# Kernel tuning notes

Hardware: AMD Instinct MI355X
Metric: run time of the kernel (lower is better)

The kernel has to match this reference:

```python
import jax, jax.numpy as jnp
import numpy as np
from jax import lax

BLOCK_SIZE = 5
GAMMA = 0.02


def setup_inputs() -> dict:
    key = jax.random.key(0)
    kx, km = jax.random.split(key)
    N, C, H, W = 64, 64, 80, 80
    x = jax.random.normal(kx, (N, C, H, W), dtype=jnp.float32)
    # Bernoulli(gamma) sample, materialized as an int32 0/1 mask (the module's
    # internal randomness, fixed for deterministic reference comparison).
    mask = (jax.random.uniform(km, (N, C, H, W)) < GAMMA).astype(jnp.int32)
    return {"x": x, "mask": mask}


def _dropblock(x, mask, block_size):
    m = mask.astype(x.dtype)  # 0/1 seed mask, shape (N,C,H,W)
    # Original scatters each seed (h,w) into [h, h+bs) x [w, w+bs) (clipped at
    # H,W). Equivalent dense form: block_mask[i,j] = max over m[i-dh, j-dw],
    # dh,dw in [0,bs) -> sliding-window max with top/left padding of bs-1.
    if block_size > 1:
        block_mask = lax.reduce_window(
            m,
            jnp.array(0.0, x.dtype),
            lax.max,
            window_dimensions=(1, 1, block_size, block_size),
            window_strides=(1, 1, 1, 1),
            padding=((0, 0), (0, 0), (block_size - 1, 0), (block_size - 1, 0)),
        )
    else:
        block_mask = m
    inv_blk_mask = 1.0 - block_mask
    countM = jnp.array(m.size, x.dtype)
    count_ones = inv_blk_mask.sum()
    return inv_blk_mask * x * (countM / count_ones)


def reference(x, mask):
    return _dropblock(x, mask, BLOCK_SIZE)
```

## Files before the change

### kernel.cpp

```cpp
#include <hip/hip_runtime.h>

#define DB_H 80
#define DB_W 80
#define DB_PLANE (DB_H * DB_W)
#define DB_NPLANES 4096
#define DB_ROW_WORDS 3
#define DB_PLANE_WORDS (DB_H * DB_ROW_WORDS)
#define DB_TOTAL (DB_PLANE * DB_NPLANES)
#define DB_COUNT_F 26214400.0f
#define DB_CNT_BYTES (DB_NPLANES * 4)
#define WPB 4

__global__ __launch_bounds__(256) void db_mask_kernel(
    const int* __restrict__ mask,
    unsigned int* __restrict__ bits,
    unsigned int* __restrict__ counts)
{
    __shared__ unsigned long long P[WPB][104];
    __shared__ unsigned int RO[WPB][DB_PLANE_WORDS];
    const int wid = threadIdx.x >> 6, lane = threadIdx.x & 63;
    const int plane = blockIdx.x * WPB + wid;
    const int* mp = mask + plane * DB_PLANE;
    unsigned long long* Pp = P[wid];
    unsigned int* ro = RO[wid];

    #pragma unroll
    for (int c = 0; c < 4; ++c) {
        int v[25];
        #pragma unroll
        for (int k = 0; k < 25; ++k) v[k] = mp[(c * 25 + k) * 64 + lane];
        #pragma unroll
        for (int k = 0; k < 25; ++k) {
            unsigned long long bal = __ballot(v[k] & 1);
            if (lane == 0) Pp[c * 25 + k] = bal;
        }
    }
    if (lane < 4) Pp[100 + lane] = 0ULL;
    __syncthreads();

    for (int r = lane; r < DB_H; r += 64) {
        const int bitpos = r * DB_W;
        const int q = bitpos >> 6, off = bitpos & 63;
        unsigned long long a, b;
        if (off) {
            a = (Pp[q] >> off) | (Pp[q + 1] << (64 - off));
            b = (Pp[q + 1] >> off) | (Pp[q + 2] << (64 - off));
        } else {
            a = Pp[q]; b = Pp[q + 1];
        }
        b &= 0xFFFFULL;
        unsigned long long ra = a, rb = b;
        #pragma unroll
        for (int s = 1; s <= 4; ++s) {
            ra |= a << s;
            rb |= (b << s) | (a >> (64 - s));
        }
        rb &= 0xFFFFULL;
        ro[r * 3 + 0] = (unsigned int)ra;
        ro[r * 3 + 1] = (unsigned int)(ra >> 32);
        ro[r * 3 + 2] = (unsigned int)rb;
    }
    __syncthreads();

    unsigned int zeros = 0;
    for (int i = lane; i < DB_H; i += 64) {
        const int lo = (i >= 4) ? i - 4 : 0;
        unsigned int c0 = 0, c1 = 0, c2 = 0;
        for (int ii = lo; ii <= i; ++ii) {
            c0 |= ro[ii * 3 + 0];
            c1 |= ro[ii * 3 + 1];
            c2 |= ro[ii * 3 + 2];
        }
        zeros += 80u - __popc(c0) - __popc(c1) - __popc(c2);
        unsigned int* bp = bits + plane * DB_PLANE_WORDS + i * 3;
        bp[0] = c0; bp[1] = c1; bp[2] = c2;
    }
    for (int off = 32; off > 0; off >>= 1)
        zeros += (unsigned int)__shfl_down((int)zeros, off, 64);
    if (lane == 0) counts[plane] = zeros;
}

__global__ __launch_bounds__(256) void db_apply_bits(
    const float4* __restrict__ x,
    const unsigned int* __restrict__ bits,
    const unsigned int* __restrict__ counts,
    float4* __restrict__ out)
{
    __shared__ float s_scale;
    __shared__ unsigned int s_part[4];
    {
        const uint4* cp = (const uint4*)counts;
        unsigned int c = 0;
        #pragma unroll
        for (int k = 0; k < 4; ++k) {
            uint4 v = cp[k * 256 + threadIdx.x];
            c += v.x + v.y + v.z + v.w;
        }
        for (int off = 32; off > 0; off >>= 1)
            c += (unsigned int)__shfl_down((int)c, off, 64);
        if ((threadIdx.x & 63) == 0) s_part[threadIdx.x >> 6] = c;
        __syncthreads();
        if (threadIdx.x == 0)
            s_scale = DB_COUNT_F /
                      (float)(s_part[0] + s_part[1] + s_part[2] + s_part[3]);
        __syncthreads();
    }
    const float scale = s_scale;
    const int NG = DB_TOTAL / 4;
    const int stride = gridDim.x * blockDim.x;
    #pragma unroll 2
    for (int g = blockIdx.x * blockDim.x + threadIdx.x; g < NG; g += stride) {
        float4 v = x[g];
        int e = g * 4;
        int plane = e / DB_PLANE;
        int ep = e - plane * DB_PLANE;
        int i = ep / DB_W;
        int j = ep - i * DB_W;
        unsigned int wb =
            bits[plane * DB_PLANE_WORDS + i * 3 + (j >> 5)] >> (j & 31);
        float4 o;
        o.x = (wb & 1u) ? 0.0f : v.x * scale;
        o.y = (wb & 2u) ? 0.0f : v.y * scale;
        o.z = (wb & 4u) ? 0.0f : v.z * scale;
        o.w = (wb & 8u) ? 0.0f : v.w * scale;
        out[g] = o;
    }
}

__global__ __launch_bounds__(256) void db_count_kernel(
    const int* __restrict__ mask,
    unsigned int* __restrict__ counts)
{
    __shared__ unsigned long long P[WPB][104];
    __shared__ unsigned int RO[WPB][DB_PLANE_WORDS];
    const int wid = threadIdx.x >> 6, lane = threadIdx.x & 63;
    const int plane = blockIdx.x * WPB + wid;
    const int* mp = mask + plane * DB_PLANE;
    unsigned long long* Pp = P[wid];
    unsigned int* ro = RO[wid];
    #pragma unroll
    for (int c = 0; c < 4; ++c) {
        int v[25];
        #pragma unroll
        for (int k = 0; k < 25; ++k) v[k] = mp[(c * 25 + k) * 64 + lane];
        #pragma unroll
        for (int k = 0; k < 25; ++k) {
            unsigned long long bal = __ballot(v[k] & 1);
            if (lane == 0) Pp[c * 25 + k] = bal;
        }
    }
    if (lane < 4) Pp[100 + lane] = 0ULL;
    __syncthreads();
    for (int r = lane; r < DB_H; r += 64) {
        const int bitpos = r * DB_W;
        const int q = bitpos >> 6, off = bitpos & 63;
        unsigned long long a, b;
        if (off) {
            a = (Pp[q] >> off) | (Pp[q + 1] << (64 - off));
            b = (Pp[q + 1] >> off) | (Pp[q + 2] << (64 - off));
        } else {
            a = Pp[q]; b = Pp[q + 1];
        }
        b &= 0xFFFFULL;
        unsigned long long ra = a, rb = b;
        #pragma unroll
        for (int s = 1; s <= 4; ++s) {
            ra |= a << s;
            rb |= (b << s) | (a >> (64 - s));
        }
        rb &= 0xFFFFULL;
        ro[r * 3 + 0] = (unsigned int)ra;
        ro[r * 3 + 1] = (unsigned int)(ra >> 32);
        ro[r * 3 + 2] = (unsigned int)rb;
    }
    __syncthreads();
    unsigned int zeros = 0;
    for (int i = lane; i < DB_H; i += 64) {
        const int lo = (i >= 4) ? i - 4 : 0;
        unsigned int c0 = 0, c1 = 0, c2 = 0;
        for (int ii = lo; ii <= i; ++ii) {
            c0 |= ro[ii * 3 + 0];
            c1 |= ro[ii * 3 + 1];
            c2 |= ro[ii * 3 + 2];
        }
        zeros += 80u - __popc(c0) - __popc(c1) - __popc(c2);
    }
    for (int off = 32; off > 0; off >>= 1)
        zeros += (unsigned int)__shfl_down((int)zeros, off, 64);
    if (lane == 0) counts[plane] = zeros;
}

__global__ __launch_bounds__(256) void db_apply_recompute(
    const float* __restrict__ x,
    const int* __restrict__ mask,
    const unsigned int* __restrict__ counts,
    float* __restrict__ out)
{
    __shared__ unsigned long long P[WPB][104];
    __shared__ unsigned int RO[WPB][DB_PLANE_WORDS];
    __shared__ unsigned int BM[WPB][DB_PLANE_WORDS];
    __shared__ float s_scale;
    __shared__ unsigned int s_part[4];
    {
        const uint4* cp = (const uint4*)counts;
        unsigned int c = 0;
        #pragma unroll
        for (int k = 0; k < 4; ++k) {
            uint4 v = cp[k * 256 + threadIdx.x];
            c += v.x + v.y + v.z + v.w;
        }
        for (int off = 32; off > 0; off >>= 1)
            c += (unsigned int)__shfl_down((int)c, off, 64);
        if ((threadIdx.x & 63) == 0) s_part[threadIdx.x >> 6] = c;
        __syncthreads();
        if (threadIdx.x == 0)
            s_scale = DB_COUNT_F /
                      (float)(s_part[0] + s_part[1] + s_part[2] + s_part[3]);
        __syncthreads();
    }
    const float scale = s_scale;
    const int wid = threadIdx.x >> 6, lane = threadIdx.x & 63;
    const int plane = blockIdx.x * WPB + wid;
    const int* mp = mask + plane * DB_PLANE;
    unsigned long long* Pp = P[wid];
    unsigned int* ro = RO[wid];
    #pragma unroll
    for (int c = 0; c < 4; ++c) {
        int v[25];
        #pragma unroll
        for (int k = 0; k < 25; ++k) v[k] = mp[(c * 25 + k) * 64 + lane];
        #pragma unroll
        for (int k = 0; k < 25; ++k) {
            unsigned long long bal = __ballot(v[k] & 1);
            if (lane == 0) Pp[c * 25 + k] = bal;
        }
    }
    if (lane < 4) Pp[100 + lane] = 0ULL;
    __syncthreads();
    for (int r = lane; r < DB_H; r += 64) {
        const int bitpos = r * DB_W;
        const int q = bitpos >> 6, off = bitpos & 63;
        unsigned long long a, b;
        if (off) {
            a = (Pp[q] >> off) | (Pp[q + 1] << (64 - off));
            b = (Pp[q + 1] >> off) | (Pp[q + 2] << (64 - off));
        } else {
            a = Pp[q]; b = Pp[q + 1];
        }
        b &= 0xFFFFULL;
        unsigned long long ra = a, rb = b;
        #pragma unroll
        for (int s = 1; s <= 4; ++s) {
            ra |= a << s;
            rb |= (b << s) | (a >> (64 - s));
        }
        rb &= 0xFFFFULL;
        ro[r * 3 + 0] = (unsigned int)ra;
        ro[r * 3 + 1] = (unsigned int)(ra >> 32);
        ro[r * 3 + 2] = (unsigned int)rb;
    }
    __syncthreads();
    unsigned int* bmp = BM[wid];
    for (int i = lane; i < DB_H; i += 64) {
        const int lo = (i >= 4) ? i - 4 : 0;
        unsigned int c0 = 0, c1 = 0, c2 = 0;
        for (int ii = lo; ii <= i; ++ii) {
            c0 |= ro[ii * 3 + 0];
            c1 |= ro[ii * 3 + 1];
            c2 |= ro[ii * 3 + 2];
        }
        bmp[i * 3 + 0] = c0; bmp[i * 3 + 1] = c1; bmp[i * 3 + 2] = c2;
    }
    __syncthreads();
    const float* xp = x + plane * DB_PLANE;
    float* op = out + plane * DB_PLANE;
    for (int e = lane; e < DB_PLANE; e += 64) {
        int i = e / DB_W, j = e - i * DB_W;
        unsigned int wb = bmp[i * 3 + (j >> 5)] >> (j & 31);
        op[e] = (wb & 1u) ? 0.0f : xp[e] * scale;
    }
}

extern "C" void kernel_launch(void* const* d_in, const int* in_sizes, int n_in,
                              void* d_out, int out_size, void* d_ws, size_t ws_size,
                              hipStream_t stream) {
    const float* x = (const float*)d_in[0];
    const int* mask = (const int*)d_in[1];
    float* out = (float*)d_out;

    unsigned int* counts = (unsigned int*)d_ws;
    unsigned int* bits = (unsigned int*)((char*)d_ws + DB_CNT_BYTES);
    const size_t bits_bytes = (size_t)DB_NPLANES * DB_PLANE_WORDS * 4;
    const bool use_bits = ws_size >= DB_CNT_BYTES + bits_bytes;

    if (use_bits) {
        db_mask_kernel<<<DB_NPLANES / WPB, 256, 0, stream>>>(mask, bits, counts);
        db_apply_bits<<<2048, 256, 0, stream>>>(
            (const float4*)x, bits, counts, (float4*)out);
    } else {
        db_count_kernel<<<DB_NPLANES / WPB, 256, 0, stream>>>(mask, counts);
        db_apply_recompute<<<DB_NPLANES / WPB, 256, 0, stream>>>(
            x, mask, counts, out);
    }
}
```

Baseline: 66.11 us.

## Split each plane across two waves and skip x loads for fully masked quads

The mask kernel now gives each plane to two wavefronts, each handling half the rows, with a shared-memory combine of the zero counts. This doubles the block count and lowers register use by shrinking the load unroll. The apply kernel skips reading x when all four elements of a float4 are masked, saving some read bandwidth. The fallback kernels also get smaller unroll chunks. The cost is an extra barrier and a divergent load in the apply loop.

```diff
diff --git a/kernel.cpp b/kernel.cpp
--- a/kernel.cpp
+++ b/kernel.cpp
@@ -9,6 +9,7 @@
 #define DB_TOTAL (DB_PLANE * DB_NPLANES)
 #define DB_COUNT_F 26214400.0f
 #define DB_CNT_BYTES (DB_NPLANES * 4)
+#define PPBLK 2
 #define WPB 4
 
 __global__ __launch_bounds__(256) void db_mask_kernel(
@@ -16,29 +17,34 @@
     unsigned int* __restrict__ bits,
     unsigned int* __restrict__ counts)
 {
-    __shared__ unsigned long long P[WPB][104];
-    __shared__ unsigned int RO[WPB][DB_PLANE_WORDS];
-    const int wid = threadIdx.x >> 6, lane = threadIdx.x & 63;
-    const int plane = blockIdx.x * WPB + wid;
+    __shared__ unsigned long long P[PPBLK][104];
+    __shared__ unsigned int RO[PPBLK][DB_PLANE_WORDS];
+    __shared__ unsigned int ZP[PPBLK][2];
+    const int t = threadIdx.x;
+    const int wid = t >> 6, lane = t & 63;
+    const int pib = wid >> 1, half = wid & 1;
+    const int plane = blockIdx.x * PPBLK + pib;
     const int* mp = mask + plane * DB_PLANE;
-    unsigned long long* Pp = P[wid];
-    unsigned int* ro = RO[wid];
-
-    #pragma unroll
-    for (int c = 0; c < 4; ++c) {
-        int v[25];
-        #pragma unroll
-        for (int k = 0; k < 25; ++k) v[k] = mp[(c * 25 + k) * 64 + lane];
-        #pragma unroll
-        for (int k = 0; k < 25; ++k) {
+    unsigned long long* Pp = P[pib];
+    unsigned int* ro = RO[pib];
+
+    #pragma unroll 1
+    for (int c = 0; c < 5; ++c) {
+        int v[10];
+        const int base = half * 50 + c * 10;
+        #pragma unroll
+        for (int k = 0; k < 10; ++k) v[k] = mp[(base + k) * 64 + lane];
+        #pragma unroll
+        for (int k = 0; k < 10; ++k) {
             unsigned long long bal = __ballot(v[k] & 1);
-            if (lane == 0) Pp[c * 25 + k] = bal;
-        }
-    }
-    if (lane < 4) Pp[100 + lane] = 0ULL;
-    __syncthreads();
-
-    for (int r = lane; r < DB_H; r += 64) {
+            if (lane == 0) Pp[base + k] = bal;
+        }
+    }
+    if (t < 2 * 4) P[t >> 2][100 + (t & 3)] = 0ULL;
+    __syncthreads();
+
+    if (lane < 40) {
+        const int r = half * 40 + lane;
         const int bitpos = r * DB_W;
         const int q = bitpos >> 6, off = bitpos & 63;
         unsigned long long a, b;
@@ -63,7 +69,8 @@
     __syncthreads();
 
     unsigned int zeros = 0;
-    for (int i = lane; i < DB_H; i += 64) {
+    if (lane < 40) {
+        const int i = half * 40 + lane;
         const int lo = (i >= 4) ? i - 4 : 0;
         unsigned int c0 = 0, c1 = 0, c2 = 0;
         for (int ii = lo; ii <= i; ++ii) {
@@ -71,13 +78,16 @@
             c1 |= ro[ii * 3 + 1];
             c2 |= ro[ii * 3 + 2];
         }
-        zeros += 80u - __popc(c0) - __popc(c1) - __popc(c2);
+        zeros = 80u - __popc(c0) - __popc(c1) - __popc(c2);
         unsigned int* bp = bits + plane * DB_PLANE_WORDS + i * 3;
         bp[0] = c0; bp[1] = c1; bp[2] = c2;
     }
     for (int off = 32; off > 0; off >>= 1)
         zeros += (unsigned int)__shfl_down((int)zeros, off, 64);
-    if (lane == 0) counts[plane] = zeros;
+    if (lane == 0) ZP[pib][half] = zeros;
+    __syncthreads();
+    if (lane == 0 && half == 0)
+        counts[plane] = ZP[pib][0] + ZP[pib][1];
 }
 
 __global__ __launch_bounds__(256) void db_apply_bits(
@@ -110,19 +120,20 @@
     const int stride = gridDim.x * blockDim.x;
     #pragma unroll 2
     for (int g = blockIdx.x * blockDim.x + threadIdx.x; g < NG; g += stride) {
-        float4 v = x[g];
         int e = g * 4;
         int plane = e / DB_PLANE;
         int ep = e - plane * DB_PLANE;
         int i = ep / DB_W;
         int j = ep - i * DB_W;
-        unsigned int wb =
-            bits[plane * DB_PLANE_WORDS + i * 3 + (j >> 5)] >> (j & 31);
+        unsigned int nib =
+            (bits[plane * DB_PLANE_WORDS + i * 3 + (j >> 5)] >> (j & 31)) & 0xFu;
+        float4 v = make_float4(0.f, 0.f, 0.f, 0.f);
+        if (nib != 0xFu) v = x[g];
         float4 o;
-        o.x = (wb & 1u) ? 0.0f : v.x * scale;
-        o.y = (wb & 2u) ? 0.0f : v.y * scale;
-        o.z = (wb & 4u) ? 0.0f : v.z * scale;
-        o.w = (wb & 8u) ? 0.0f : v.w * scale;
+        o.x = (nib & 1u) ? 0.0f : v.x * scale;
+        o.y = (nib & 2u) ? 0.0f : v.y * scale;
+        o.z = (nib & 4u) ? 0.0f : v.z * scale;
+        o.w = (nib & 8u) ? 0.0f : v.w * scale;
         out[g] = o;
     }
 }
@@ -138,15 +149,15 @@
     const int* mp = mask + plane * DB_PLANE;
     unsigned long long* Pp = P[wid];
     unsigned int* ro = RO[wid];
-    #pragma unroll
-    for (int c = 0; c < 4; ++c) {
-        int v[25];
-        #pragma unroll
-        for (int k = 0; k < 25; ++k) v[k] = mp[(c * 25 + k) * 64 + lane];
-        #pragma unroll
-        for (int k = 0; k < 25; ++k) {
+    #pragma unroll 1
+    for (int c = 0; c < 10; ++c) {
+        int v[10];
+        #pragma unroll
+        for (int k = 0; k < 10; ++k) v[k] = mp[(c * 10 + k) * 64 + lane];
+        #pragma unroll
+        for (int k = 0; k < 10; ++k) {
             unsigned long long bal = __ballot(v[k] & 1);
-            if (lane == 0) Pp[c * 25 + k] = bal;
+            if (lane == 0) Pp[c * 10 + k] = bal;
         }
     }
     if (lane < 4) Pp[100 + lane] = 0ULL;
@@ -224,15 +235,15 @@
     const int* mp = mask + plane * DB_PLANE;
     unsigned long long* Pp = P[wid];
     unsigned int* ro = RO[wid];
-    #pragma unroll
-    for (int c = 0; c < 4; ++c) {
-        int v[25];
-        #pragma unroll
-        for (int k = 0; k < 25; ++k) v[k] = mp[(c * 25 + k) * 64 + lane];
-        #pragma unroll
-        for (int k = 0; k < 25; ++k) {
+    #pragma unroll 1
+    for (int c = 0; c < 10; ++c) {
+        int v[10];
+        #pragma unroll
+        for (int k = 0; k < 10; ++k) v[k] = mp[(c * 10 + k) * 64 + lane];
+        #pragma unroll
+        for (int k = 0; k < 10; ++k) {
             unsigned long long bal = __ballot(v[k] & 1);
-            if (lane == 0) Pp[c * 25 + k] = bal;
+            if (lane == 0) Pp[c * 10 + k] = bal;
         }
     }
     if (lane < 4) Pp[100 + lane] = 0ULL;
@@ -294,7 +305,7 @@
     const bool use_bits = ws_size >= DB_CNT_BYTES + bits_bytes;
 
     if (use_bits) {
-        db_mask_kernel<<<DB_NPLANES / WPB, 256, 0, stream>>>(mask, bits, counts);
+        db_mask_kernel<<<DB_NPLANES / PPBLK, 256, 0, stream>>>(mask, bits, counts);
         db_apply_bits<<<2048, 256, 0, stream>>>(
             (const float4*)x, bits, counts, (float4*)out);
     } else {
```

After: 65.11 us. About the same (-1.5%).
